# Kernel optimization log

Measured on AMD Instinct MI355X. Metric: run time of the kernel, lower is better.

Reference implementation:

```python
import jax, jax.numpy as jnp
import numpy as np

N, E, F, H, B = 100000, 600000, 128, 128, 250


def setup_inputs() -> dict:
    key = jax.random.key(0)
    ks = jax.random.split(key, 10)
    x = jax.random.normal(ks[0], (N, F), dtype=jnp.float32)
    # last two columns encode cluster id c in {0,1,2}: c = x[:,-1] + 2*x[:,-2]
    c = jax.random.randint(ks[1], (N,), 0, 3)
    x = x.at[:, -2].set((c == 2).astype(jnp.float32))
    x = x.at[:, -1].set((c == 1).astype(jnp.float32))
    edge_index = jax.random.randint(ks[2], (2, E), 0, N, dtype=jnp.int64)
    batch = (jnp.arange(N, dtype=jnp.int64) // (N // B))  # 400 nodes per graph
    s = 1.0 / np.sqrt(F)
    sh = 1.0 / np.sqrt(H)
    W1 = jax.random.uniform(ks[3], (F, H), jnp.float32, -s, s)
    b1 = jnp.zeros((H,), jnp.float32)
    W2 = jax.random.uniform(ks[4], (H, H), jnp.float32, -sh, sh)
    b2 = jnp.zeros((H,), jnp.float32)
    W3 = jax.random.uniform(ks[5], (H, H), jnp.float32, -sh, sh)
    b3 = jnp.zeros((H,), jnp.float32)
    sl = 1.0 / np.sqrt(3 * H)
    Wl = jax.random.uniform(ks[6], (3 * H, 1), jnp.float32, -sl, sl)
    bl = jax.random.uniform(ks[7], (1,), jnp.float32, -sl, sl)
    return {"x": x, "edge_index": edge_index, "batch": batch,
            "W1": W1, "b1": b1, "W2": W2, "b2": b2, "W3": W3, "b3": b3,
            "Wl": Wl, "bl": bl}


def _gcn_conv(h, W, b, src, dst, dinv):
    # PyG GCNConv: h @ W, then D^{-1/2} (A + I) D^{-1/2} aggregation, + bias.
    h = h @ W
    norm = dinv[src] * dinv[dst]              # [E+N]
    msg = h[src] * norm[:, None]              # gather + scale
    out = jax.ops.segment_sum(msg, dst, num_segments=N)  # scatter-add at target
    return out + b


def _forward(x, edge_index, batch, W1, b1, W2, b2, W3, b3, Wl, bl):
    cluster = (x[:, -1] + 2.0 * x[:, -2]).astype(jnp.int64)  # in {0,1,2}
    loop = jnp.arange(N, dtype=edge_index.dtype)
    src = jnp.concatenate([edge_index[0], loop])  # self-loops appended
    dst = jnp.concatenate([edge_index[1], loop])
    deg = jax.ops.segment_sum(jnp.ones_like(dst, dtype=x.dtype), dst, num_segments=N)
    dinv = jax.lax.rsqrt(jnp.maximum(deg, 1.0))  # deg >= 1 via self-loops

    h = jax.nn.relu(_gcn_conv(x, W1, b1, src, dst, dinv))
    h = jax.nn.relu(_gcn_conv(h, W2, b2, src, dst, dinv))
    h = _gcn_conv(h, W3, b3, src, dst, dinv)

    cb = batch * 3 + cluster                   # segment id per (graph, cluster)
    sums = jax.ops.segment_sum(h, cb, num_segments=B * 3)
    cnts = jax.ops.segment_sum(jnp.ones((N,), h.dtype), cb, num_segments=B * 3)
    xc = sums / jnp.maximum(cnts, 1.0)[:, None]  # scatter-mean
    z = xc.reshape(B, 3 * H)                   # dropout p=0.2 is identity in eval
    return jax.nn.sigmoid(z @ Wl + bl)


def reference(x, edge_index, batch, W1, b1, W2, b2, W3, b3, Wl, bl):
    return _forward(x, edge_index, batch, W1, b1, W2, b2, W3, b3, Wl, bl)
```

## Files before the change

### kernel.cpp

```cpp
#include <hip/hip_runtime.h>
#include <hip/hip_bf16.h>
#include <math.h>


#define WAVE 64
#define NPARTS 25
#define WPADB 144
#define ELLK 32

typedef __attribute__((ext_vector_type(4))) float f32x4;
typedef __attribute__((ext_vector_type(2))) float f32x2;

__device__ __forceinline__ unsigned short bf16r(float f) {
    unsigned u = __float_as_uint(f);
    return (unsigned short)((u + 0x7fffu + ((u >> 16) & 1u)) >> 16);
}
__device__ __forceinline__ unsigned pack_fp8x4(float a, float b, float c, float d) {
    unsigned u = (unsigned)__builtin_amdgcn_cvt_pk_fp8_f32(a, b, 0, false);
    u = (unsigned)__builtin_amdgcn_cvt_pk_fp8_f32(c, d, (int)u, true);
    return u;
}
__device__ __forceinline__ void fma8_fp8(float* acc, float w, uint2 u) {
    f32x2 p0 = __builtin_amdgcn_cvt_pk_f32_fp8((int)u.x, false);
    f32x2 p1 = __builtin_amdgcn_cvt_pk_f32_fp8((int)u.x, true);
    f32x2 p2 = __builtin_amdgcn_cvt_pk_f32_fp8((int)u.y, false);
    f32x2 p3 = __builtin_amdgcn_cvt_pk_f32_fp8((int)u.y, true);
    acc[0] += w * p0.x; acc[1] += w * p0.y;
    acc[2] += w * p1.x; acc[3] += w * p1.y;
    acc[4] += w * p2.x; acc[5] += w * p2.y;
    acc[6] += w * p3.x; acc[7] += w * p3.y;
}

__device__ __forceinline__ void agg_node(const uint2* __restrict__ hb2,
                                         const int* __restrict__ deg,
                                         const int* __restrict__ ce,
                                         int nc, bool ok, int sl, float* acc) {
    uint2 self = hb2[(size_t)nc * 16 + sl];
    for (int j = 0; j < 8; ++j) acc[j] = 0.f;
    fma8_fp8(acc, 1.f, self);
    int dg = ok ? min(deg[nc], ELLK) : 0;
    const int base = nc * ELLK;
    int c0, c1, c2, c3, c4, c5, c6, c7;
    if (dg > 0) {
        int dm = dg - 1;
        c0 = ce[base];
        c1 = ce[base + min(1, dm)];
        c2 = ce[base + min(2, dm)];
        c3 = ce[base + min(3, dm)];
        c4 = ce[base + min(4, dm)];
        c5 = ce[base + min(5, dm)];
        c6 = ce[base + min(6, dm)];
        c7 = ce[base + min(7, dm)];
    }
    for (int i = 0; i < dg; i += 8) {
        int p0 = c0, p1 = c1, p2 = c2, p3 = c3;
        int p4 = c4, p5 = c5, p6 = c6, p7 = c7;
        int nx = i + 8;
        if (nx < dg) {
            int dm = dg - 1;
            c0 = ce[base + nx];
            c1 = ce[base + min(nx + 1, dm)];
            c2 = ce[base + min(nx + 2, dm)];
            c3 = ce[base + min(nx + 3, dm)];
            c4 = ce[base + min(nx + 4, dm)];
            c5 = ce[base + min(nx + 5, dm)];
            c6 = ce[base + min(nx + 6, dm)];
            c7 = ce[base + min(nx + 7, dm)];
        }
        uint2 u0 = hb2[(size_t)p0 * 16 + sl];
        uint2 u1 = hb2[(size_t)p1 * 16 + sl];
        uint2 u2 = hb2[(size_t)p2 * 16 + sl];
        uint2 u3 = hb2[(size_t)p3 * 16 + sl];
        uint2 u4 = hb2[(size_t)p4 * 16 + sl];
        uint2 u5 = hb2[(size_t)p5 * 16 + sl];
        uint2 u6 = hb2[(size_t)p6 * 16 + sl];
        uint2 u7 = hb2[(size_t)p7 * 16 + sl];
        float w1 = (i + 1 < dg) ? 1.f : 0.f;
        float w2 = (i + 2 < dg) ? 1.f : 0.f;
        float w3 = (i + 3 < dg) ? 1.f : 0.f;
        float w4 = (i + 4 < dg) ? 1.f : 0.f;
        float w5 = (i + 5 < dg) ? 1.f : 0.f;
        float w6 = (i + 6 < dg) ? 1.f : 0.f;
        float w7 = (i + 7 < dg) ? 1.f : 0.f;
        fma8_fp8(acc, 1.f, u0);
        fma8_fp8(acc, w1, u1);
        fma8_fp8(acc, w2, u2);
        fma8_fp8(acc, w3, u3);
        fma8_fp8(acc, w4, u4);
        fma8_fp8(acc, w5, u5);
        fma8_fp8(acc, w6, u6);
        fma8_fp8(acc, w7, u7);
    }
}


__global__ void fill_ell(const int* __restrict__ src, const int* __restrict__ dst,
                         int* __restrict__ deg, int* __restrict__ ce, int ne,
                         const float* __restrict__ W1, const float* __restrict__ W2,
                         const float* __restrict__ W3, const float* __restrict__ Wl,
                         unsigned* __restrict__ Wt, float* __restrict__ wv,
                         int fb) {
    int b = blockIdx.x;
    int t = threadIdx.x;
    if (b < fb) {
        int e = b * 256 + t;
        if (e < ne) {
            int d = dst[e], s = src[e];
            int slot = atomicAdd(&deg[d], 1);
            if (slot < ELLK) ce[d * ELLK + slot] = s;
        }
        return;
    }
    int p = b - fb;
    if (p < 32) {
        int layer = p >> 4;
        int idx = (p & 15) * 256 + t;
        const float* W = (layer == 0) ? W1 : W2;
        int n = idx >> 5, k4 = (idx & 31) * 4;
        float a = W[(k4 + 0) * 128 + n];
        float bb = W[(k4 + 1) * 128 + n];
        float c = W[(k4 + 2) * 128 + n];
        float d = W[(k4 + 3) * 128 + n];
        Wt[layer * 4096 + n * 32 + (idx & 31)] = pack_fp8x4(a, bb, c, d);
    } else {
        int idx = (p - 32) * 256 + t;
        if (idx < 384) {
            int c = idx >> 7, k = idx & 127;
            const float* wlc = Wl + c * 128;
            const float* w3r = W3 + k * 128;
            float s = 0.f;
#pragma unroll 8
            for (int n = 0; n < 128; ++n) s += w3r[n] * wlc[n];
            wv[c * 128 + k] = s;
        }
    }
}


__global__ void prep_kernel(const float* __restrict__ x, unsigned* __restrict__ hb,
                            const int* __restrict__ deg, float* __restrict__ dinv,
                            int* __restrict__ cluster, int n32) {
    int i = blockIdx.x * blockDim.x + threadIdx.x;
    if (i >= n32) return;
    int row = i >> 5;
    float di = rsqrtf((float)(deg[row] + 1));
    float4 v = ((const float4*)x)[i];
    hb[i] = pack_fp8x4(di * v.x, di * v.y, di * v.z, di * v.w);
    if ((i & 31) == 31) {
        dinv[row] = di;
        cluster[row] = (int)(v.w + 2.0f * v.z + 0.5f);
    }
}


__global__ void agg_kernel(const uint2* __restrict__ hb2, uint2* __restrict__ out2,
                           const int* __restrict__ deg, const int* __restrict__ ce,
                           const float* __restrict__ dinv, int n) {
    int wid = blockIdx.x * (blockDim.x >> 6) + (threadIdx.x >> 6);
    int lane = threadIdx.x & 63;
    int g = lane >> 4, sl = lane & 15;
    int node = wid * 4 + g;
    bool ok = node < n;
    int nc = ok ? node : (n - 1);
    float acc[8];
    agg_node(hb2, deg, ce, nc, ok, sl, acc);
    if (ok) {
        float di = dinv[nc];
        uint2 o;
        o.x = pack_fp8x4(di * acc[0], di * acc[1], di * acc[2], di * acc[3]);
        o.y = pack_fp8x4(di * acc[4], di * acc[5], di * acc[6], di * acc[7]);
        out2[(size_t)node * 16 + sl] = o;
    }
}


__global__ __launch_bounds__(256) void agg_pool(
    const uint2* __restrict__ hb2,
    const int* __restrict__ deg, const int* __restrict__ ce,
    const float* __restrict__ dinv, const int* __restrict__ cluster,
    float* __restrict__ psums, int* __restrict__ pcnts, int n) {
    __shared__ float smW[4][3][128];
    __shared__ int smC[4][3];
    const int t = threadIdx.x;
    for (int i = t; i < 4 * 3 * 128; i += 256) ((float*)smW)[i] = 0.f;
    if (t < 12) ((int*)smC)[t] = 0;
    __syncthreads();

    const int wave = t >> 6, lane = t & 63;
    const int g = lane >> 4, sl = lane & 15;
    const int node = blockIdx.x * 16 + wave * 4 + g;
    const bool ok = node < n;
    const int nc = ok ? node : (n - 1);
    float acc[8];
    agg_node(hb2, deg, ce, nc, ok, sl, acc);
    const float di = ok ? dinv[nc] : 0.f;

    const int cl = ok ? cluster[nc] : 0;
#pragma unroll
    for (int g2 = 0; g2 < 4; ++g2) {
        if (g == g2 && ok) {
            float* dstp = &smW[wave][cl][sl * 8];
#pragma unroll
            for (int j = 0; j < 8; ++j) dstp[j] += di * acc[j];
            if (sl == 0) smC[wave][cl] += 1;
        }
    }
    __syncthreads();

    if (t < 128) {
#pragma unroll
        for (int c = 0; c < 3; ++c) {
            float s = smW[0][c][t] + smW[1][c][t] + smW[2][c][t] + smW[3][c][t];
            psums[((size_t)blockIdx.x * 3 + c) * 128 + t] = s;
        }
    }
    if (t < 3)
        pcnts[blockIdx.x * 3 + t] = smC[0][t] + smC[1][t] + smC[2][t] + smC[3][t];
}


__global__ __launch_bounds__(256) void gemm_mfma(const unsigned char* __restrict__ A,
                                                 const unsigned char* __restrict__ Wt,
                                                 const float* __restrict__ bias,
                                                 const float* __restrict__ dinv,
                                                 unsigned char* __restrict__ Cb,
                                                 int n) {
    __shared__ unsigned char sm[128 * WPADB];
    const int t = threadIdx.x;
    const int wave = t >> 6, lane = t & 63;
    const int quad = lane >> 4, lr = lane & 15;
    const size_t row0 = (size_t)blockIdx.x * 128 + wave * 32;

    {
        int r = t >> 1, h = t & 1;
        const uint4* s = (const uint4*)(Wt + r * 128 + h * 64);
        uint4* d = (uint4*)(sm + r * WPADB + h * 64);
#pragma unroll
        for (int i = 0; i < 4; ++i) d[i] = s[i];
    }
    __syncthreads();

    f32x4 acc[2][8];
#pragma unroll
    for (int i2 = 0; i2 < 2; ++i2)
#pragma unroll
        for (int ct = 0; ct < 8; ++ct) acc[i2][ct] = (f32x4){0.f, 0.f, 0.f, 0.f};

    const unsigned char* arow0 = A + (row0 + lr) * 128;
    const unsigned char* arow1 = arow0 + 16 * 128;
#pragma unroll
    for (int kc = 0; kc < 4; ++kc) {
        int kb = kc * 32 + quad * 8;
        long a0 = *(const long*)(arow0 + kb);
        long a1 = *(const long*)(arow1 + kb);
#pragma unroll
        for (int ct = 0; ct < 8; ++ct) {
            long w = *(const long*)(sm + (ct * 16 + lr) * WPADB + kb);
            acc[0][ct] = __builtin_amdgcn_mfma_f32_16x16x32_fp8_fp8(w, a0, acc[0][ct], 0, 0, 0);
            acc[1][ct] = __builtin_amdgcn_mfma_f32_16x16x32_fp8_fp8(w, a1, acc[1][ct], 0, 0, 0);
        }
    }

#pragma unroll
    for (int i2 = 0; i2 < 2; ++i2) {
        int row = (int)row0 + i2 * 16 + lr;
        float di = (row < n) ? dinv[row] : 0.f;
        unsigned char* crow = Cb + (size_t)row * 128;
#pragma unroll
        for (int ct = 0; ct < 8; ++ct) {
            float4 bq = *(const float4*)&bias[ct * 16 + quad * 4];
            float v0 = di * fmaxf(acc[i2][ct][0] + bq.x, 0.f);
            float v1 = di * fmaxf(acc[i2][ct][1] + bq.y, 0.f);
            float v2 = di * fmaxf(acc[i2][ct][2] + bq.z, 0.f);
            float v3 = di * fmaxf(acc[i2][ct][3] + bq.w, 0.f);
            *(unsigned*)(crow + ct * 16 + quad * 4) = pack_fp8x4(v0, v1, v2, v3);
        }
    }
}

__global__ void head_kernel(const float* __restrict__ part_sums,
                            const int* __restrict__ part_cnts,
                            const float* __restrict__ wv, const float* __restrict__ b3,
                            const float* __restrict__ Wl, const float* __restrict__ bl,
                            float* __restrict__ out) {
    int b = blockIdx.x, t = threadIdx.x;
    float s0 = 0.f, s1 = 0.f, s2 = 0.f;
    int n0 = 0, n1 = 0, n2 = 0;
#pragma unroll
    for (int p = 0; p < NPARTS; ++p) {
        int blk = b * NPARTS + p;
        size_t o = (size_t)blk * 384 + t;
        s0 += part_sums[o];
        s1 += part_sums[o + 128];
        s2 += part_sums[o + 256];
        n0 += part_cnts[blk * 3 + 0];
        n1 += part_cnts[blk * 3 + 1];
        n2 += part_cnts[blk * 3 + 2];
    }
    float bt = b3[t];
    float z = 0.f;
    if (n0 > 0) z += (s0 / (float)n0) * wv[t]       + bt * Wl[t];
    if (n1 > 0) z += (s1 / (float)n1) * wv[128 + t] + bt * Wl[128 + t];
    if (n2 > 0) z += (s2 / (float)n2) * wv[256 + t] + bt * Wl[256 + t];
    for (int off = 32; off > 0; off >>= 1) z += __shfl_down(z, off);
    __shared__ float partial[2];
    if ((t & 63) == 0) partial[t >> 6] = z;
    __syncthreads();
    if (t == 0) {
        float zz = partial[0] + partial[1] + bl[0];
        out[b] = 1.0f / (1.0f + expf(-zz));
    }
}


extern "C" void kernel_launch(void* const* d_in, const int* in_sizes, int n_in,
                              void* d_out, int out_size, void* d_ws, size_t ws_size,
                              hipStream_t stream) {
    const float* x  = (const float*)d_in[0];
    const int*   ei = (const int*)d_in[1];
    const float* W1 = (const float*)d_in[3];
    const float* b1 = (const float*)d_in[4];
    const float* W2 = (const float*)d_in[5];
    const float* b2 = (const float*)d_in[6];
    const float* W3 = (const float*)d_in[7];
    const float* b3 = (const float*)d_in[8];
    const float* Wl = (const float*)d_in[9];
    const float* bl = (const float*)d_in[10];
    float* out = (float*)d_out;

    const int N = in_sizes[0] / 128;
    const int E = in_sizes[1] / 2;
    const int B = out_size;
    const int Npad = (N + 127) & ~127;

    const int* srcp = ei;
    const int* dstp = ei + E;

    char* ws = (char*)d_ws;
    size_t off = 0;
    auto alloc = [&](size_t bytes) -> char* {
        char* p = ws + off;
        off += (bytes + 255) & ~(size_t)255;
        return p;
    };
    unsigned char*  hb = (unsigned char*) alloc((size_t)Npad * 128);
    unsigned char*  ab = (unsigned char*) alloc((size_t)Npad * 128);
    unsigned*       wt = (unsigned*)      alloc((size_t)2 * 4096 * 4);
    float* wv      = (float*)alloc(384 * 4);
    float* dinv    = (float*)alloc((size_t)N * 4);
    int*   cluster = (int*)  alloc((size_t)N * 4);
    int*   ce      = (int*)  alloc((size_t)N * ELLK * 4);
    float* psums   = (float*)alloc((size_t)B * NPARTS * 3 * 128 * 4);
    int*   pcnts   = (int*)  alloc((size_t)B * NPARTS * 3 * 4);
    int*   deg     = (int*)  alloc((size_t)N * 4);
    (void)ws_size; (void)n_in;

    hipMemsetAsync(deg, 0, (size_t)N * 4, stream);

    int fb = (E + 255) / 256;
    fill_ell<<<fb + 34, 256, 0, stream>>>(srcp, dstp, deg, ce, E,
                                          W1, W2, W3, Wl, wt, wv, fb);
    prep_kernel<<<(N * 32 + 255) / 256, 256, 0, stream>>>(x, (unsigned*)hb, deg,
                                                          dinv, cluster, N * 32);

    int gemmBlocks = Npad / 128;
    int aggBlocks = (N + 15) / 16;

    agg_kernel<<<aggBlocks, 256, 0, stream>>>((const uint2*)hb, (uint2*)ab,
                                              deg, ce, dinv, N);
    gemm_mfma<<<gemmBlocks, 256, 0, stream>>>(ab, (const unsigned char*)wt,
                                              b1, dinv, hb, N);
    agg_kernel<<<aggBlocks, 256, 0, stream>>>((const uint2*)hb, (uint2*)ab,
                                              deg, ce, dinv, N);
    gemm_mfma<<<gemmBlocks, 256, 0, stream>>>(ab, (const unsigned char*)wt + 16384,
                                              b2, dinv, hb, N);

    agg_pool<<<aggBlocks, 256, 0, stream>>>((const uint2*)hb, deg, ce,
                                            dinv, cluster, psums, pcnts, N);
    head_kernel<<<B, 128, 0, stream>>>(psums, pcnts, wv, b3, Wl, bl, out);
}
```

Measured before the change: 249.1 us.

## Merge prep into edge-fill kernel and apply source normalization in first aggregation

Folds the x-to-fp8 conversion into the ELL-building kernel, so one launch both scatters edges and quantizes features. This breaks the dependency on final degrees at prep time, so the first aggregation now computes each neighbor's rsqrt(deg+1) on the fly. The dinv array is removed and recomputed from deg everywhere, and edge scattering is vectorized to four edges per thread. In exchange the first aggregation does extra per-neighbor degree gathers, and fp8 quantization of unscaled x slightly changes numerics.

```diff
diff --git a/kernel.cpp b/kernel.cpp
--- a/kernel.cpp
+++ b/kernel.cpp
@@ -94,24 +94,41 @@
 }
 
 
-__global__ void fill_ell(const int* __restrict__ src, const int* __restrict__ dst,
-                         int* __restrict__ deg, int* __restrict__ ce, int ne,
-                         const float* __restrict__ W1, const float* __restrict__ W2,
-                         const float* __restrict__ W3, const float* __restrict__ Wl,
-                         unsigned* __restrict__ Wt, float* __restrict__ wv,
-                         int fb) {
+__global__ void mega_prep(const int* __restrict__ src, const int* __restrict__ dst,
+                          int* __restrict__ deg, int* __restrict__ ce, int ne,
+                          const float* __restrict__ W1, const float* __restrict__ W2,
+                          const float* __restrict__ W3, const float* __restrict__ Wl,
+                          unsigned* __restrict__ Wt, float* __restrict__ wv,
+                          const float* __restrict__ x, unsigned* __restrict__ hb,
+                          int* __restrict__ cluster, int n32, int eb) {
     int b = blockIdx.x;
     int t = threadIdx.x;
-    if (b < fb) {
-        int e = b * 256 + t;
-        if (e < ne) {
-            int d = dst[e], s = src[e];
-            int slot = atomicAdd(&deg[d], 1);
-            if (slot < ELLK) ce[d * ELLK + slot] = s;
+    if (b < eb) {
+        int e4 = b * 256 + t;
+        int e = e4 * 4;
+        if (e + 3 < ne) {
+            int4 d4 = ((const int4*)dst)[e4];
+            int4 s4 = ((const int4*)src)[e4];
+            int sl0 = atomicAdd(&deg[d4.x], 1);
+            if (sl0 < ELLK) ce[d4.x * ELLK + sl0] = s4.x;
+            int sl1 = atomicAdd(&deg[d4.y], 1);
+            if (sl1 < ELLK) ce[d4.y * ELLK + sl1] = s4.y;
+            int sl2 = atomicAdd(&deg[d4.z], 1);
+            if (sl2 < ELLK) ce[d4.z * ELLK + sl2] = s4.z;
+            int sl3 = atomicAdd(&deg[d4.w], 1);
+            if (sl3 < ELLK) ce[d4.w * ELLK + sl3] = s4.w;
+        } else {
+            for (int k = 0; k < 4; ++k) {
+                if (e + k < ne) {
+                    int d = dst[e + k], s = src[e + k];
+                    int slot = atomicAdd(&deg[d], 1);
+                    if (slot < ELLK) ce[d * ELLK + slot] = s;
+                }
+            }
         }
         return;
     }
-    int p = b - fb;
+    int p = b - eb;
     if (p < 32) {
         int layer = p >> 4;
         int idx = (p & 15) * 256 + t;
@@ -122,7 +139,7 @@
         float c = W[(k4 + 2) * 128 + n];
         float d = W[(k4 + 3) * 128 + n];
         Wt[layer * 4096 + n * 32 + (idx & 31)] = pack_fp8x4(a, bb, c, d);
-    } else {
+    } else if (p < 34) {
         int idx = (p - 32) * 256 + t;
         if (idx < 384) {
             int c = idx >> 7, k = idx & 127;
@@ -133,29 +150,79 @@
             for (int n = 0; n < 128; ++n) s += w3r[n] * wlc[n];
             wv[c * 128 + k] = s;
         }
-    }
-}
-
-
-__global__ void prep_kernel(const float* __restrict__ x, unsigned* __restrict__ hb,
-                            const int* __restrict__ deg, float* __restrict__ dinv,
-                            int* __restrict__ cluster, int n32) {
-    int i = blockIdx.x * blockDim.x + threadIdx.x;
-    if (i >= n32) return;
-    int row = i >> 5;
-    float di = rsqrtf((float)(deg[row] + 1));
-    float4 v = ((const float4*)x)[i];
-    hb[i] = pack_fp8x4(di * v.x, di * v.y, di * v.z, di * v.w);
-    if ((i & 31) == 31) {
-        dinv[row] = di;
-        cluster[row] = (int)(v.w + 2.0f * v.z + 0.5f);
+    } else {
+        int i = (p - 34) * 256 + t;
+        if (i < n32) {
+            float4 v = ((const float4*)x)[i];
+            hb[i] = pack_fp8x4(v.x, v.y, v.z, v.w);
+            if ((i & 31) == 31)
+                cluster[i >> 5] = (int)(v.w + 2.0f * v.z + 0.5f);
+        }
+    }
+}
+
+
+__global__ void agg1_kernel(const uint2* __restrict__ hb2, uint2* __restrict__ out2,
+                            const int* __restrict__ deg, const int* __restrict__ ce,
+                            int n) {
+    int wid = blockIdx.x * (blockDim.x >> 6) + (threadIdx.x >> 6);
+    int lane = threadIdx.x & 63;
+    int g = lane >> 4, sl = lane & 15;
+    int node = wid * 4 + g;
+    bool ok = node < n;
+    int nc = ok ? node : (n - 1);
+    int dgc = deg[nc];
+    float dd = rsqrtf((float)(dgc + 1));
+    uint2 self = hb2[(size_t)nc * 16 + sl];
+    float acc[8];
+    for (int j = 0; j < 8; ++j) acc[j] = 0.f;
+    fma8_fp8(acc, dd, self);
+    int dg = ok ? min(dgc, ELLK) : 0;
+    const int base = nc * ELLK;
+    int c0, c1, c2, c3;
+    if (dg > 0) {
+        int dm = dg - 1;
+        c0 = ce[base];
+        c1 = ce[base + min(1, dm)];
+        c2 = ce[base + min(2, dm)];
+        c3 = ce[base + min(3, dm)];
+    }
+    for (int i = 0; i < dg; i += 4) {
+        int p0 = c0, p1 = c1, p2 = c2, p3 = c3;
+        int nx = i + 4;
+        if (nx < dg) {
+            int dm = dg - 1;
+            c0 = ce[base + nx];
+            c1 = ce[base + min(nx + 1, dm)];
+            c2 = ce[base + min(nx + 2, dm)];
+            c3 = ce[base + min(nx + 3, dm)];
+        }
+        uint2 u0 = hb2[(size_t)p0 * 16 + sl];
+        uint2 u1 = hb2[(size_t)p1 * 16 + sl];
+        uint2 u2 = hb2[(size_t)p2 * 16 + sl];
+        uint2 u3 = hb2[(size_t)p3 * 16 + sl];
+        int d0 = deg[p0], d1 = deg[p1], d2 = deg[p2], d3 = deg[p3];
+        float w0 = rsqrtf((float)(d0 + 1));
+        float w1 = (i + 1 < dg) ? rsqrtf((float)(d1 + 1)) : 0.f;
+        float w2 = (i + 2 < dg) ? rsqrtf((float)(d2 + 1)) : 0.f;
+        float w3 = (i + 3 < dg) ? rsqrtf((float)(d3 + 1)) : 0.f;
+        fma8_fp8(acc, w0, u0);
+        fma8_fp8(acc, w1, u1);
+        fma8_fp8(acc, w2, u2);
+        fma8_fp8(acc, w3, u3);
+    }
+    if (ok) {
+        uint2 o;
+        o.x = pack_fp8x4(dd * acc[0], dd * acc[1], dd * acc[2], dd * acc[3]);
+        o.y = pack_fp8x4(dd * acc[4], dd * acc[5], dd * acc[6], dd * acc[7]);
+        out2[(size_t)node * 16 + sl] = o;
     }
 }
 
 
 __global__ void agg_kernel(const uint2* __restrict__ hb2, uint2* __restrict__ out2,
                            const int* __restrict__ deg, const int* __restrict__ ce,
-                           const float* __restrict__ dinv, int n) {
+                           int n) {
     int wid = blockIdx.x * (blockDim.x >> 6) + (threadIdx.x >> 6);
     int lane = threadIdx.x & 63;
     int g = lane >> 4, sl = lane & 15;
@@ -165,7 +232,7 @@
     float acc[8];
     agg_node(hb2, deg, ce, nc, ok, sl, acc);
     if (ok) {
-        float di = dinv[nc];
+        float di = rsqrtf((float)(deg[nc] + 1));
         uint2 o;
         o.x = pack_fp8x4(di * acc[0], di * acc[1], di * acc[2], di * acc[3]);
         o.y = pack_fp8x4(di * acc[4], di * acc[5], di * acc[6], di * acc[7]);
@@ -177,7 +244,7 @@
 __global__ __launch_bounds__(256) void agg_pool(
     const uint2* __restrict__ hb2,
     const int* __restrict__ deg, const int* __restrict__ ce,
-    const float* __restrict__ dinv, const int* __restrict__ cluster,
+    const int* __restrict__ cluster,
     float* __restrict__ psums, int* __restrict__ pcnts, int n) {
     __shared__ float smW[4][3][128];
     __shared__ int smC[4][3];
@@ -193,7 +260,7 @@
     const int nc = ok ? node : (n - 1);
     float acc[8];
     agg_node(hb2, deg, ce, nc, ok, sl, acc);
-    const float di = ok ? dinv[nc] : 0.f;
+    const float di = ok ? rsqrtf((float)(deg[nc] + 1)) : 0.f;
 
     const int cl = ok ? cluster[nc] : 0;
 #pragma unroll
@@ -222,7 +289,7 @@
 __global__ __launch_bounds__(256) void gemm_mfma(const unsigned char* __restrict__ A,
                                                  const unsigned char* __restrict__ Wt,
                                                  const float* __restrict__ bias,
-                                                 const float* __restrict__ dinv,
+                                                 const int* __restrict__ deg,
                                                  unsigned char* __restrict__ Cb,
                                                  int n) {
     __shared__ unsigned char sm[128 * WPADB];
@@ -264,7 +331,7 @@
 #pragma unroll
     for (int i2 = 0; i2 < 2; ++i2) {
         int row = (int)row0 + i2 * 16 + lr;
-        float di = (row < n) ? dinv[row] : 0.f;
+        float di = (row < n) ? rsqrtf((float)(deg[row] + 1)) : 0.f;
         unsigned char* crow = Cb + (size_t)row * 128;
 #pragma unroll
         for (int ct = 0; ct < 8; ++ct) {
@@ -347,7 +414,6 @@
     unsigned char*  ab = (unsigned char*) alloc((size_t)Npad * 128);
     unsigned*       wt = (unsigned*)      alloc((size_t)2 * 4096 * 4);
     float* wv      = (float*)alloc(384 * 4);
-    float* dinv    = (float*)alloc((size_t)N * 4);
     int*   cluster = (int*)  alloc((size_t)N * 4);
     int*   ce      = (int*)  alloc((size_t)N * ELLK * 4);
     float* psums   = (float*)alloc((size_t)B * NPARTS * 3 * 128 * 4);
@@ -357,25 +423,27 @@
 
     hipMemsetAsync(deg, 0, (size_t)N * 4, stream);
 
-    int fb = (E + 255) / 256;
-    fill_ell<<<fb + 34, 256, 0, stream>>>(srcp, dstp, deg, ce, E,
-                                          W1, W2, W3, Wl, wt, wv, fb);
-    prep_kernel<<<(N * 32 + 255) / 256, 256, 0, stream>>>(x, (unsigned*)hb, deg,
-                                                          dinv, cluster, N * 32);
+    const int eb = ((E + 3) / 4 + 255) / 256;
+    const int n32 = N * 32;
+    const int pb = (n32 + 255) / 256;
+    mega_prep<<<eb + 34 + pb, 256, 0, stream>>>(srcp, dstp, deg, ce, E,
+                                                W1, W2, W3, Wl, wt, wv,
+                                                x, (unsigned*)hb, cluster,
+                                                n32, eb);
 
     int gemmBlocks = Npad / 128;
     int aggBlocks = (N + 15) / 16;
 
+    agg1_kernel<<<aggBlocks, 256, 0, stream>>>((const uint2*)hb, (uint2*)ab,
+                                               deg, ce, N);
+    gemm_mfma<<<gemmBlocks, 256, 0, stream>>>(ab, (const unsigned char*)wt,
+                                              b1, deg, hb, N);
     agg_kernel<<<aggBlocks, 256, 0, stream>>>((const uint2*)hb, (uint2*)ab,
-                                              deg, ce, dinv, N);
-    gemm_mfma<<<gemmBlocks, 256, 0, stream>>>(ab, (const unsigned char*)wt,
-                                              b1, dinv, hb, N);
-    agg_kernel<<<aggBlocks, 256, 0, stream>>>((const uint2*)hb, (uint2*)ab,
-                                              deg, ce, dinv, N);
+                                              deg, ce, N);
     gemm_mfma<<<gemmBlocks, 256, 0, stream>>>(ab, (const unsigned char*)wt + 16384,
-                                              b2, dinv, hb, N);
+                                              b2, deg, hb, N);
 
     agg_pool<<<aggBlocks, 256, 0, stream>>>((const uint2*)hb, deg, ce,
-                                            dinv, cluster, psums, pcnts, N);
+                                            cluster, psums, pcnts, N);
     head_kernel<<<B, 128, 0, stream>>>(psums, pcnts, wv, b3, Wl, bl, out);
 }
```

New measurement: 255.5 us. +2.6%, slower.
